# Kernel tuning notes

Measured on AMD Instinct MI355X. Metric: run time of the kernel, lower is better.

The kernel has to match this reference:

```python
import jax, jax.numpy as jnp
import numpy as np

B, E, F, T, RANK, L = 8, 512, 1024, 2048, 10, 5


def setup_inputs() -> dict:
    key = jax.random.key(0)
    ks = jax.random.split(key, 6)
    Y = jax.random.normal(ks[0], (B, E, T), dtype=jnp.float32)
    R = jax.random.uniform(ks[1], (B, E, F), dtype=jnp.float32)
    Omega = (jax.random.uniform(ks[2], (B, E, T)) < 0.9).astype(jnp.float32)
    P0 = jax.random.normal(ks[3], (B, E, RANK), dtype=jnp.float32)
    Q0 = jax.random.normal(ks[4], (B, T, RANK), dtype=jnp.float32)
    A0 = jnp.zeros((B, F, T), dtype=jnp.float32)
    lam_log = jnp.full((L,), -5.0, dtype=jnp.float32)   # init_val=-5
    mu_log = jnp.full((L,), -5.0, dtype=jnp.float32)
    skip_logits = jnp.full((L, 3), 0.5, dtype=jnp.float32)  # skip_P, skip_Q, skip_A
    return {"Y": Y, "R": R, "Omega": Omega, "P0": P0, "Q0": Q0, "A0": A0,
            "lam_log": lam_log, "mu_log": mu_log, "skip_logits": skip_logits}


def _soft(x, t):
    return jnp.sign(x) * jnp.maximum(jnp.abs(x) - t, 0.0)


def _forward(Y, R, Omega, P0, Q0, A0, lam_log, mu_log, skip_logits):
    r = P0.shape[-1]
    I = jnp.eye(r, dtype=Y.dtype)

    def step(carry, params):
        P, Q, A = carry
        ll, ml, sk = params
        lam = jnp.exp(ll)   # lam1 == lam2 (two_lambda=False)
        mu = jnp.exp(ml)
        err = Omega * (Y - R @ A)                                   # [B,E,T]
        # --- P update: per-row masked ridge solve ---
        Mp = jnp.einsum('bet,btr,bts->bers', Omega, Q, Q) + lam * I  # [B,E,r,r]
        rhsP = jnp.einsum('bet,btr->ber', err, Q)
        P_hat = jnp.linalg.solve(Mp, rhsP[..., None])[..., 0]
        P_new = P + jax.nn.sigmoid(sk[0]) * (P_hat - P)
        # --- Q update: per-column masked ridge solve (uses P_new, same err) ---
        Mq = jnp.einsum('bet,ber,bes->btrs', Omega, P_new, P_new) + lam * I
        rhsQ = jnp.einsum('bet,ber->btr', err, P_new)
        Q_hat = jnp.linalg.solve(Mq, rhsQ[..., None])[..., 0]
        Q_new = Q + jax.nn.sigmoid(sk[1]) * (Q_hat - Q)
        # --- A update: soft-thresholded BSCA step ---
        datafit = Omega * (Y - P_new @ jnp.swapaxes(Q_new, -2, -1) - R @ A)
        A_scale = jnp.einsum('bef,bet->bft', R * R, Omega)          # [B,F,T]
        BA_temp = A_scale * A + jnp.einsum('bef,bet->bft', R, datafit)
        zero = A_scale == 0
        denom = jnp.where(zero, 1.0, A_scale)
        A_hat = jnp.where(zero, 0.0, _soft(BA_temp, mu) / denom)
        A_new = A + jax.nn.sigmoid(sk[2]) * (A_hat - A)
        return (P_new, Q_new, A_new), None

    (P, Q, A), _ = jax.lax.scan(step, (P0, Q0, A0), (lam_log, mu_log, skip_logits))
    return P, Q, A


def reference(Y, R, Omega, P0, Q0, A0, lam_log, mu_log, skip_logits):
    return _forward(Y, R, Omega, P0, Q0, A0, lam_log, mu_log, skip_logits)
```

## Files before the change

kernel.cpp:

```cpp
#include <hip/hip_runtime.h>

constexpr int B_ = 8, E_ = 512, F_ = 1024, T_ = 2048, R_ = 10, L_ = 5;
constexpr int NTRI = 55;
constexpr int BM_ = 128, BN_ = 256, BK_ = 32;

enum { EPI_STORE = 0, EPI_ERR = 1, EPI_AUPD = 2, EPI_AUPD0 = 3 };

typedef __attribute__((ext_vector_type(4))) float f32x4;
typedef __attribute__((ext_vector_type(8))) short short8v;
union U8 { unsigned u[4]; short8v s; };

__device__ __forceinline__ unsigned bf16r(float v) {
  unsigned u = __float_as_uint(v);
  return (u + 0x7fffu + ((u >> 16) & 1u)) >> 16;
}
__device__ __forceinline__ unsigned pack1(float v) {
  unsigned h = bf16r(v);
  float lo = v - __uint_as_float(h << 16);
  return h | (bf16r(lo) << 16);
}
__device__ __forceinline__ uint4 pack4(float4 v) {
  uint4 r;
  r.x = pack1(v.x); r.y = pack1(v.y); r.z = pack1(v.z); r.w = pack1(v.w);
  return r;
}
__device__ __forceinline__ void unpack8(uint4 w0, uint4 w1, U8& hi, U8& lo) {
  hi.u[0] = __builtin_amdgcn_perm(w0.y, w0.x, 0x05040100u);
  lo.u[0] = __builtin_amdgcn_perm(w0.y, w0.x, 0x07060302u);
  hi.u[1] = __builtin_amdgcn_perm(w0.w, w0.z, 0x05040100u);
  lo.u[1] = __builtin_amdgcn_perm(w0.w, w0.z, 0x07060302u);
  hi.u[2] = __builtin_amdgcn_perm(w1.y, w1.x, 0x05040100u);
  lo.u[2] = __builtin_amdgcn_perm(w1.y, w1.x, 0x07060302u);
  hi.u[3] = __builtin_amdgcn_perm(w1.w, w1.z, 0x05040100u);
  lo.u[3] = __builtin_amdgcn_perm(w1.w, w1.z, 0x07060302u);
}

__device__ __forceinline__ float sigmoidf_(float v) {
  return 1.0f / (1.0f + expf(-v));
}

__device__ __forceinline__ void solve10(float M[NTRI], const float rhs[R_],
                                        float lam, float x[R_]) {
#pragma unroll
  for (int j = 0; j < R_; j++) M[j * (j + 1) / 2 + j] += lam;
#pragma unroll
  for (int j = 0; j < R_; j++) {
    float s = M[j * (j + 1) / 2 + j];
#pragma unroll
    for (int k = 0; k < j; k++) {
      float l = M[j * (j + 1) / 2 + k];
      s -= l * l;
    }
    s = fmaxf(s, 1e-30f);
    float d = sqrtf(s);
    float inv = 1.0f / d;
    M[j * (j + 1) / 2 + j] = d;
#pragma unroll
    for (int i = j + 1; i < R_; i++) {
      float s2 = M[i * (i + 1) / 2 + j];
#pragma unroll
      for (int k = 0; k < j; k++)
        s2 -= M[i * (i + 1) / 2 + k] * M[j * (j + 1) / 2 + k];
      M[i * (i + 1) / 2 + j] = s2 * inv;
    }
  }
  float y[R_];
#pragma unroll
  for (int i = 0; i < R_; i++) {
    float s = rhs[i];
#pragma unroll
    for (int k = 0; k < i; k++) s -= M[i * (i + 1) / 2 + k] * y[k];
    y[i] = s / M[i * (i + 1) / 2 + i];
  }
#pragma unroll
  for (int ii = R_ - 1; ii >= 0; ii--) {
    float s = y[ii];
#pragma unroll
    for (int k = ii + 1; k < R_; k++) s -= M[k * (k + 1) / 2 + ii] * x[k];
    x[ii] = s / M[ii * (ii + 1) / 2 + ii];
  }
}

template <int MODE>
__global__ __launch_bounds__(256) void trans_k(const float* __restrict__ in0,
                                               const float* __restrict__ in1,
                                               float* __restrict__ out, int Rw,
                                               int Cl) {
  __shared__ float tile[32][36];
  long ib = (long)blockIdx.z * Rw * Cl;
  int r0 = blockIdx.y * 32, c0 = blockIdx.x * 32;
  int tid = threadIdx.x;
  int c4 = (tid & 7) << 2, r = tid >> 3;
  float4 v = *(const float4*)(in0 + ib + (long)(r0 + r) * Cl + c0 + c4);
  if (MODE == 1) {
    float4 w = *(const float4*)(in1 + ib + (long)(r0 + r) * Cl + c0 + c4);
    v.x *= w.x; v.y *= w.y; v.z *= w.z; v.w *= w.w;
  }
  *(float4*)&tile[r][c4] = v;
  __syncthreads();
  int co = tid >> 3, ro4 = (tid & 7) << 2;
  float4 o;
  o.x = tile[ro4 + 0][co];
  o.y = tile[ro4 + 1][co];
  o.z = tile[ro4 + 2][co];
  o.w = tile[ro4 + 3][co];
  *(float4*)(out + ib + (long)(c0 + co) * Rw + r0 + ro4) = o;
}

template <int EPI, int SQB>
__global__ __launch_bounds__(256, 2) void gemm_split(
    const float* __restrict__ Ag, const float* __restrict__ Bg,
    float* __restrict__ Cg, const float* __restrict__ aux1,
    const float* __restrict__ aux2, const float* __restrict__ mu_log,
    const float* __restrict__ sk, int step, int M, int N, int K, long sA,
    long sB, long sC) {
  __shared__ unsigned As[BM_ * BK_];
  __shared__ unsigned Bs[BN_ * BK_];
  int b = blockIdx.z;
  const float* A = Ag + (long)b * sA;
  const float* Bop = Bg + (long)b * sB;
  float* C = Cg + (long)b * sC;
  const float* x1 = aux1 ? aux1 + (long)b * sC : nullptr;
  const float* x2 = aux2 ? aux2 + (long)b * sC : nullptr;

  int tid = threadIdx.x;
  int m0 = blockIdx.y * BM_, n0 = blockIdx.x * BN_;
  int g = tid & 7, rb = tid >> 3;
  int g4 = g << 2;
  int l = tid & 63, lr = l & 15, lh = l >> 4;
  int wv = tid >> 6, wr = wv >> 1, wc = wv & 1;

  f32x4 acc[4][8];
#pragma unroll
  for (int i = 0; i < 4; i++)
#pragma unroll
    for (int j = 0; j < 8; j++) acc[i][j] = {0.f, 0.f, 0.f, 0.f};

  float4 va[4], vb[8];
#pragma unroll
  for (int p = 0; p < 4; p++)
    va[p] = *(const float4*)&A[(long)(m0 + rb + 32 * p) * K + g4];
#pragma unroll
  for (int p = 0; p < 8; p++)
    vb[p] = *(const float4*)&Bop[(long)(n0 + rb + 32 * p) * K + g4];

  for (int kt = 0; kt < K; kt += BK_) {
    uint4 pa[4], pb[8];
#pragma unroll
    for (int p = 0; p < 4; p++) pa[p] = pack4(va[p]);
#pragma unroll
    for (int p = 0; p < 8; p++) {
      float4 v = vb[p];
      if (SQB) { v.x *= v.x; v.y *= v.y; v.z *= v.z; v.w *= v.w; }
      pb[p] = pack4(v);
    }
    __syncthreads();
#pragma unroll
    for (int p = 0; p < 4; p++) {
      int row = rb + 32 * p;
      *(uint4*)&As[row * BK_ + ((g ^ (row & 7)) << 2)] = pa[p];
    }
#pragma unroll
    for (int p = 0; p < 8; p++) {
      int row = rb + 32 * p;
      *(uint4*)&Bs[row * BK_ + ((g ^ (row & 7)) << 2)] = pb[p];
    }
    __syncthreads();
    if (kt + BK_ < K) {
#pragma unroll
      for (int p = 0; p < 4; p++)
        va[p] = *(const float4*)&A[(long)(m0 + rb + 32 * p) * K + kt + BK_ + g4];
#pragma unroll
      for (int p = 0; p < 8; p++)
        vb[p] = *(const float4*)&Bop[(long)(n0 + rb + 32 * p) * K + kt + BK_ + g4];
    }
    U8 aH[4], aL[4];
#pragma unroll
    for (int mf = 0; mf < 4; mf++) {
      int m = wr * 64 + mf * 16 + lr;
      int s7 = m & 7, g0 = 2 * lh;
      uint4 w0 = *(const uint4*)&As[m * BK_ + ((g0 ^ s7) << 2)];
      uint4 w1 = *(const uint4*)&As[m * BK_ + (((g0 + 1) ^ s7) << 2)];
      unpack8(w0, w1, aH[mf], aL[mf]);
    }
#pragma unroll
    for (int nf = 0; nf < 8; nf++) {
      int n = wc * 128 + nf * 16 + lr;
      int s7 = n & 7, g0 = 2 * lh;
      uint4 w0 = *(const uint4*)&Bs[n * BK_ + ((g0 ^ s7) << 2)];
      uint4 w1 = *(const uint4*)&Bs[n * BK_ + (((g0 + 1) ^ s7) << 2)];
      U8 bH, bL;
      unpack8(w0, w1, bH, bL);
#pragma unroll
      for (int mf = 0; mf < 4; mf++) {
        acc[mf][nf] = __builtin_amdgcn_mfma_f32_16x16x32_bf16(
            aH[mf].s, bH.s, acc[mf][nf], 0, 0, 0);
        acc[mf][nf] = __builtin_amdgcn_mfma_f32_16x16x32_bf16(
            aL[mf].s, bH.s, acc[mf][nf], 0, 0, 0);
        acc[mf][nf] = __builtin_amdgcn_mfma_f32_16x16x32_bf16(
            aH[mf].s, bL.s, acc[mf][nf], 0, 0, 0);
      }
    }
  }

  float mu = 0.f, s2 = 0.f;
  if (EPI == EPI_AUPD || EPI == EPI_AUPD0) {
    mu = expf(mu_log[step]);
    s2 = sigmoidf_(sk[step * 3 + 2]);
  }
#pragma unroll
  for (int mf = 0; mf < 4; mf++) {
#pragma unroll
    for (int nf = 0; nf < 8; nf++) {
#pragma unroll
      for (int r = 0; r < 4; r++) {
        int m = m0 + wr * 64 + mf * 16 + lh * 4 + r;
        int n = n0 + wc * 128 + nf * 16 + lr;
        long idx = (long)m * N + n;
        float c = acc[mf][nf][r];
        if (EPI == EPI_STORE) {
          C[idx] = c;
        } else if (EPI == EPI_ERR) {
          C[idx] = x1[idx] - x2[idx] * c;
        } else {
          float asv = x1[idx];
          float aold = (EPI == EPI_AUPD) ? C[idx] : 0.f;
          float bat = fmaf(asv, aold, c);
          float mag = fmaxf(fabsf(bat) - mu, 0.f);
          float sft = copysignf(mag, bat);
          float ahat = (asv == 0.f) ? 0.f : sft / asv;
          C[idx] = aold + s2 * (ahat - aold);
        }
      }
    }
  }
}

__global__ __launch_bounds__(256) void p_stage1(const float* __restrict__ errT,
                                                const float* __restrict__ OmT,
                                                const float* __restrict__ Q,
                                                float* __restrict__ scr) {
  int tc = blockIdx.x, eb = blockIdx.y, b = blockIdx.z;
  int e = eb * 256 + threadIdx.x;
  float Ms[NTRI], rhs[R_];
#pragma unroll
  for (int i = 0; i < NTRI; i++) Ms[i] = 0.f;
#pragma unroll
  for (int i = 0; i < R_; i++) rhs[i] = 0.f;
  long base = (long)b * T_ * E_ + e;
  for (int t = tc * 128; t < tc * 128 + 128; ++t) {
    const float* qr = Q + ((long)b * T_ + t) * R_;
    float q[R_];
#pragma unroll
    for (int r = 0; r < R_; r++) q[r] = qr[r];
    float w = OmT[base + (long)t * E_];
    float ev = errT[base + (long)t * E_];
    float wq[R_];
#pragma unroll
    for (int r = 0; r < R_; r++) {
      wq[r] = w * q[r];
      rhs[r] = fmaf(ev, q[r], rhs[r]);
    }
    int idx = 0;
#pragma unroll
    for (int r = 0; r < R_; r++)
#pragma unroll
      for (int s = 0; s <= r; s++) {
        Ms[idx] = fmaf(wq[r], q[s], Ms[idx]);
        idx++;
      }
  }
  long so = ((long)b * 16 + tc) * 65 * E_ + e;
#pragma unroll
  for (int i = 0; i < NTRI; i++) scr[so + (long)i * E_] = Ms[i];
#pragma unroll
  for (int i = 0; i < R_; i++) scr[so + (long)(NTRI + i) * E_] = rhs[i];
}

__global__ __launch_bounds__(256) void p_stage2(
    const float* __restrict__ scr, const float* __restrict__ Pin,
    float* __restrict__ Pout, const float* __restrict__ lam_log,
    const float* __restrict__ sk, int step) {
  int idx = blockIdx.x * 256 + threadIdx.x;
  int b = idx >> 9, e = idx & 511;
  float Ms[NTRI], rhs[R_], x[R_];
#pragma unroll
  for (int i = 0; i < NTRI; i++) Ms[i] = 0.f;
#pragma unroll
  for (int i = 0; i < R_; i++) rhs[i] = 0.f;
  for (int tc = 0; tc < 16; ++tc) {
    long so = ((long)b * 16 + tc) * 65 * E_ + e;
#pragma unroll
    for (int i = 0; i < NTRI; i++) Ms[i] += scr[so + (long)i * E_];
#pragma unroll
    for (int i = 0; i < R_; i++) rhs[i] += scr[so + (long)(NTRI + i) * E_];
  }
  float lam = expf(lam_log[step]);
  solve10(Ms, rhs, lam, x);
  float s0 = sigmoidf_(sk[step * 3 + 0]);
#pragma unroll
  for (int r = 0; r < R_; r++) {
    float pold = Pin[(long)idx * R_ + r];
    Pout[(long)idx * R_ + r] = pold + s0 * (x[r] - pold);
  }
}

__global__ __launch_bounds__(256) void q_stage1(const float* __restrict__ errT,
                                                const float* __restrict__ OmT,
                                                const float* __restrict__ Pn,
                                                float* __restrict__ scr) {
  int ec = blockIdx.x, tb = blockIdx.y, b = blockIdx.z;
  int t = tb * 256 + threadIdx.x;
  float Ms[NTRI], rhs[R_];
#pragma unroll
  for (int i = 0; i < NTRI; i++) Ms[i] = 0.f;
#pragma unroll
  for (int i = 0; i < R_; i++) rhs[i] = 0.f;
  long base = ((long)b * T_ + t) * E_;
  for (int e = ec * 128; e < ec * 128 + 128; ++e) {
    const float* pr = Pn + ((long)b * E_ + e) * R_;
    float p[R_];
#pragma unroll
    for (int r = 0; r < R_; r++) p[r] = pr[r];
    float w = OmT[base + e];
    float ev = errT[base + e];
    float wp[R_];
#pragma unroll
    for (int r = 0; r < R_; r++) {
      wp[r] = w * p[r];
      rhs[r] = fmaf(ev, p[r], rhs[r]);
    }
    int idx = 0;
#pragma unroll
    for (int r = 0; r < R_; r++)
#pragma unroll
      for (int s = 0; s <= r; s++) {
        Ms[idx] = fmaf(wp[r], p[s], Ms[idx]);
        idx++;
      }
  }
  long so = ((long)b * 4 + ec) * 65 * T_ + t;
#pragma unroll
  for (int i = 0; i < NTRI; i++) scr[so + (long)i * T_] = Ms[i];
#pragma unroll
  for (int i = 0; i < R_; i++) scr[so + (long)(NTRI + i) * T_] = rhs[i];
}

__global__ __launch_bounds__(256) void q_stage2(
    const float* __restrict__ scr, const float* __restrict__ Qin,
    float* __restrict__ Qout, const float* __restrict__ lam_log,
    const float* __restrict__ sk, int step) {
  int idx = blockIdx.x * 256 + threadIdx.x;
  int b = idx >> 11, t = idx & 2047;
  float Ms[NTRI], rhs[R_], x[R_];
#pragma unroll
  for (int i = 0; i < NTRI; i++) Ms[i] = 0.f;
#pragma unroll
  for (int i = 0; i < R_; i++) rhs[i] = 0.f;
  for (int ec = 0; ec < 4; ++ec) {
    long so = ((long)b * 4 + ec) * 65 * T_ + t;
#pragma unroll
    for (int i = 0; i < NTRI; i++) Ms[i] += scr[so + (long)i * T_];
#pragma unroll
    for (int i = 0; i < R_; i++) rhs[i] += scr[so + (long)(NTRI + i) * T_];
  }
  float lam = expf(lam_log[step]);
  solve10(Ms, rhs, lam, x);
  float s1 = sigmoidf_(sk[step * 3 + 1]);
#pragma unroll
  for (int r = 0; r < R_; r++) {
    float qold = Qin[(long)idx * R_ + r];
    Qout[(long)idx * R_ + r] = qold + s1 * (x[r] - qold);
  }
}

__global__ __launch_bounds__(256) void datafit_k(
    const float* __restrict__ errIn, float* __restrict__ errOut,
    const float* __restrict__ OmT, const float* __restrict__ Pn,
    const float* __restrict__ Qn) {
  int tc = blockIdx.x, eb = blockIdx.y, b = blockIdx.z;
  int e = eb * 256 + threadIdx.x;
  float p[R_];
#pragma unroll
  for (int r = 0; r < R_; r++) p[r] = Pn[((long)b * E_ + e) * R_ + r];
  for (int t = tc * 16; t < tc * 16 + 16; ++t) {
    const float* qr = Qn + ((long)b * T_ + t) * R_;
    float dot = 0.f;
#pragma unroll
    for (int r = 0; r < R_; r++) dot = fmaf(p[r], qr[r], dot);
    long ix = ((long)b * T_ + t) * E_ + e;
    errOut[ix] = errIn[ix] - OmT[ix] * dot;
  }
}

extern "C" void kernel_launch(void* const* d_in, const int* in_sizes, int n_in,
                              void* d_out, int out_size, void* d_ws,
                              size_t ws_size, hipStream_t stream) {
  const float* Y = (const float*)d_in[0];
  const float* Rm = (const float*)d_in[1];
  const float* Om = (const float*)d_in[2];
  const float* P0 = (const float*)d_in[3];
  const float* Q0 = (const float*)d_in[4];
  const float* lam_log = (const float*)d_in[6];
  const float* mu_log = (const float*)d_in[7];
  const float* sk = (const float*)d_in[8];

  float* ws = (float*)d_ws;
  float* OmT = ws;
  float* YOm = OmT + (long)B_ * T_ * E_;
  float* errT = YOm + (long)B_ * T_ * E_;
  float* AscT = errT + (long)B_ * T_ * E_;
  float* Rt = AscT + (long)B_ * T_ * F_;
  float* Pa = Rt + (long)B_ * F_ * E_;
  float* Pb = Pa + B_ * E_ * R_;
  float* Qa = Pb + B_ * E_ * R_;
  float* Qb = Qa + B_ * T_ * R_;
  float* scr = Qb + B_ * T_ * R_;

  float* outP = (float*)d_out;
  float* outQ = outP + B_ * E_ * R_;
  float* AT = outQ + B_ * T_ * R_;

  const float* Pr[L_] = {P0, Pa, Pb, Pa, Pb};
  float* Pw[L_] = {Pa, Pb, Pa, Pb, outP};
  const float* Qr[L_] = {Q0, Qa, Qb, Qa, Qb};
  float* Qw[L_] = {Qa, Qb, Qa, Qb, outQ};

  dim3 blk(256);
  trans_k<0><<<dim3(T_ / 32, E_ / 32, B_), blk, 0, stream>>>(Om, nullptr, OmT,
                                                             E_, T_);
  trans_k<1><<<dim3(T_ / 32, E_ / 32, B_), blk, 0, stream>>>(Y, Om, YOm, E_,
                                                             T_);
  trans_k<0><<<dim3(F_ / 32, E_ / 32, B_), blk, 0, stream>>>(Rm, nullptr, Rt,
                                                             E_, F_);
  gemm_split<EPI_STORE, 1><<<dim3(F_ / BN_, T_ / BM_, B_), blk, 0, stream>>>(
      OmT, Rt, AscT, nullptr, nullptr, nullptr, nullptr, 0, T_, F_, E_,
      (long)T_ * E_, (long)F_ * E_, (long)T_ * F_);

  for (int s = 0; s < L_; ++s) {
    const float* errS = (s == 0) ? YOm : errT;
    if (s > 0) {
      gemm_split<EPI_ERR, 0><<<dim3(E_ / BN_, T_ / BM_, B_), blk, 0, stream>>>(
          AT, Rm, errT, YOm, OmT, nullptr, nullptr, s, T_, E_, F_,
          (long)T_ * F_, (long)E_ * F_, (long)T_ * E_);
    }
    p_stage1<<<dim3(16, 2, B_), blk, 0, stream>>>(errS, OmT, Qr[s], scr);
    p_stage2<<<16, blk, 0, stream>>>(scr, Pr[s], Pw[s], lam_log, sk, s);
    q_stage1<<<dim3(4, 8, B_), blk, 0, stream>>>(errS, OmT, Pw[s], scr);
    q_stage2<<<64, blk, 0, stream>>>(scr, Qr[s], Qw[s], lam_log, sk, s);
    datafit_k<<<dim3(128, 2, B_), blk, 0, stream>>>(errS, errT, OmT, Pw[s],
                                                    Qw[s]);
    if (s == 0)
      gemm_split<EPI_AUPD0, 0>
          <<<dim3(F_ / BN_, T_ / BM_, B_), blk, 0, stream>>>(
              errT, Rt, AT, AscT, nullptr, mu_log, sk, s, T_, F_, E_,
              (long)T_ * E_, (long)F_ * E_, (long)T_ * F_);
    else
      gemm_split<EPI_AUPD, 0><<<dim3(F_ / BN_, T_ / BM_, B_), blk, 0, stream>>>(
          errT, Rt, AT, AscT, nullptr, mu_log, sk, s, T_, F_, E_,
          (long)T_ * E_, (long)F_ * E_, (long)T_ * F_);
  }
  for (int b = 0; b < B_; ++b) {
    trans_k<0><<<dim3(F_ / 32, T_ / 32, 1), blk, 0, stream>>>(
        AT + (long)b * T_ * F_, nullptr, scr, T_, F_);
    hipMemcpyAsync(AT + (long)b * T_ * F_, scr, (long)T_ * F_ * sizeof(float),
                   hipMemcpyDeviceToDevice, stream);
  }
}
```

Before: 2.423 ms.

## Store operands as pre-split bf16 hi/lo pairs and bitpack the mask

Replaces the fp32 workspaces with precomputed bf16 hi/lo split arrays for Y, err, R, R^T, R^2 and A. The GEMMs then load ready-made MFMA fragments and skip per-tile packing. Omega is bitpacked and A_scale is recomputed inside the A-update GEMM as an extra MFMA accumulation, so the A_scale buffer is gone. The final per-batch transpose plus memcpy becomes a single transpose kernel. This cuts memory traffic and conversion work, at the cost of extra MFMAs per tile and storing A with reduced-precision hi/lo.

After: 3.793 ms. 56.6% more time.

```diff
diff --git a/kernel.cpp b/kernel.cpp
--- a/kernel.cpp
+++ b/kernel.cpp
@@ -2,39 +2,24 @@
 
 constexpr int B_ = 8, E_ = 512, F_ = 1024, T_ = 2048, R_ = 10, L_ = 5;
 constexpr int NTRI = 55;
-constexpr int BM_ = 128, BN_ = 256, BK_ = 32;
-
-enum { EPI_STORE = 0, EPI_ERR = 1, EPI_AUPD = 2, EPI_AUPD0 = 3 };
+constexpr int EW = E_ / 32;
 
 typedef __attribute__((ext_vector_type(4))) float f32x4;
 typedef __attribute__((ext_vector_type(8))) short short8v;
-union U8 { unsigned u[4]; short8v s; };
-
-__device__ __forceinline__ unsigned bf16r(float v) {
+
+__device__ __forceinline__ float bf2f(unsigned short h) {
+  return __uint_as_float(((unsigned)h) << 16);
+}
+__device__ __forceinline__ unsigned short f2bf(float v) {
   unsigned u = __float_as_uint(v);
-  return (u + 0x7fffu + ((u >> 16) & 1u)) >> 16;
-}
-__device__ __forceinline__ unsigned pack1(float v) {
-  unsigned h = bf16r(v);
-  float lo = v - __uint_as_float(h << 16);
-  return h | (bf16r(lo) << 16);
-}
-__device__ __forceinline__ uint4 pack4(float4 v) {
-  uint4 r;
-  r.x = pack1(v.x); r.y = pack1(v.y); r.z = pack1(v.z); r.w = pack1(v.w);
-  return r;
-}
-__device__ __forceinline__ void unpack8(uint4 w0, uint4 w1, U8& hi, U8& lo) {
-  hi.u[0] = __builtin_amdgcn_perm(w0.y, w0.x, 0x05040100u);
-  lo.u[0] = __builtin_amdgcn_perm(w0.y, w0.x, 0x07060302u);
-  hi.u[1] = __builtin_amdgcn_perm(w0.w, w0.z, 0x05040100u);
-  lo.u[1] = __builtin_amdgcn_perm(w0.w, w0.z, 0x07060302u);
-  hi.u[2] = __builtin_amdgcn_perm(w1.y, w1.x, 0x05040100u);
-  lo.u[2] = __builtin_amdgcn_perm(w1.y, w1.x, 0x07060302u);
-  hi.u[3] = __builtin_amdgcn_perm(w1.w, w1.z, 0x05040100u);
-  lo.u[3] = __builtin_amdgcn_perm(w1.w, w1.z, 0x07060302u);
-}
-
+  u = u + 0x7fffu + ((u >> 16) & 1u);
+  return (unsigned short)(u >> 16);
+}
+__device__ __forceinline__ void split2(float v, unsigned short& h,
+                                       unsigned short& l) {
+  h = f2bf(v);
+  l = f2bf(v - bf2f(h));
+}
 __device__ __forceinline__ float sigmoidf_(float v) {
   return 1.0f / (1.0f + expf(-v));
 }
@@ -81,22 +66,551 @@
   }
 }
 
-template <int MODE>
-__global__ __launch_bounds__(256) void trans_k(const float* __restrict__ in0,
-                                               const float* __restrict__ in1,
-                                               float* __restrict__ out, int Rw,
-                                               int Cl) {
-  __shared__ float tile[32][36];
-  long ib = (long)blockIdx.z * Rw * Cl;
-  int r0 = blockIdx.y * 32, c0 = blockIdx.x * 32;
+__global__ __launch_bounds__(256, 2) void gemm_err(
+    const unsigned short* __restrict__ AHp, const unsigned short* __restrict__ ALp,
+    const unsigned short* __restrict__ BHp, const unsigned short* __restrict__ BLp,
+    const unsigned short* __restrict__ YHp, const unsigned short* __restrict__ YLp,
+    const unsigned* __restrict__ omb, unsigned short* __restrict__ eHp,
+    unsigned short* __restrict__ eLp) {
+  constexpr int K = F_;
+  __shared__ unsigned short AsH[4096], AsL[4096], BsH[4096], BsL[4096];
+  int b = blockIdx.z, tid = threadIdx.x;
+  int m0 = blockIdx.y * 128, n0 = blockIdx.x * 128;
+  const unsigned short* AH = AHp + (long)b * T_ * F_;
+  const unsigned short* AL = ALp + (long)b * T_ * F_;
+  const unsigned short* BH = BHp + (long)b * E_ * F_;
+  const unsigned short* BL = BLp + (long)b * E_ * F_;
+  int lr = tid & 15, lh = (tid >> 4) & 3, wv = tid >> 6, wr = wv >> 1,
+      wc = wv & 1;
+  int srow = tid >> 2, sslot = tid & 3;
+
+  f32x4 acc[4][4];
+#pragma unroll
+  for (int i = 0; i < 4; i++)
+#pragma unroll
+    for (int j = 0; j < 4; j++) acc[i][j] = {0.f, 0.f, 0.f, 0.f};
+
+  uint4 ld[8];
+#pragma unroll
+  for (int j = 0; j < 2; j++) {
+    ld[j] = *(const uint4*)&AH[(long)(m0 + srow + 64 * j) * K + sslot * 8];
+    ld[2 + j] = *(const uint4*)&AL[(long)(m0 + srow + 64 * j) * K + sslot * 8];
+    ld[4 + j] = *(const uint4*)&BH[(long)(n0 + srow + 64 * j) * K + sslot * 8];
+    ld[6 + j] = *(const uint4*)&BL[(long)(n0 + srow + 64 * j) * K + sslot * 8];
+  }
+  for (int kt = 0; kt < K; kt += 32) {
+#pragma unroll
+    for (int j = 0; j < 2; j++) {
+      int li = (srow + 64 * j) * 32 + sslot * 8;
+      *(uint4*)&AsH[li] = ld[j];
+      *(uint4*)&AsL[li] = ld[2 + j];
+      *(uint4*)&BsH[li] = ld[4 + j];
+      *(uint4*)&BsL[li] = ld[6 + j];
+    }
+    __syncthreads();
+    if (kt + 32 < K) {
+      int k1 = kt + 32;
+#pragma unroll
+      for (int j = 0; j < 2; j++) {
+        ld[j] = *(const uint4*)&AH[(long)(m0 + srow + 64 * j) * K + k1 + sslot * 8];
+        ld[2 + j] = *(const uint4*)&AL[(long)(m0 + srow + 64 * j) * K + k1 + sslot * 8];
+        ld[4 + j] = *(const uint4*)&BH[(long)(n0 + srow + 64 * j) * K + k1 + sslot * 8];
+        ld[6 + j] = *(const uint4*)&BL[(long)(n0 + srow + 64 * j) * K + k1 + sslot * 8];
+      }
+    }
+    short8v aH[4], aL[4];
+#pragma unroll
+    for (int mf = 0; mf < 4; mf++) {
+      int ml = wr * 64 + mf * 16 + lr;
+      aH[mf] = *(const short8v*)&AsH[ml * 32 + lh * 8];
+      aL[mf] = *(const short8v*)&AsL[ml * 32 + lh * 8];
+    }
+#pragma unroll
+    for (int nf = 0; nf < 4; nf++) {
+      int nl = wc * 64 + nf * 16 + lr;
+      short8v bH = *(const short8v*)&BsH[nl * 32 + lh * 8];
+      short8v bL = *(const short8v*)&BsL[nl * 32 + lh * 8];
+#pragma unroll
+      for (int mf = 0; mf < 4; mf++) {
+        acc[mf][nf] = __builtin_amdgcn_mfma_f32_16x16x32_bf16(aH[mf], bH,
+                                                              acc[mf][nf], 0, 0, 0);
+        acc[mf][nf] = __builtin_amdgcn_mfma_f32_16x16x32_bf16(aH[mf], bL,
+                                                              acc[mf][nf], 0, 0, 0);
+        acc[mf][nf] = __builtin_amdgcn_mfma_f32_16x16x32_bf16(aL[mf], bH,
+                                                              acc[mf][nf], 0, 0, 0);
+      }
+    }
+    __syncthreads();
+  }
+#pragma unroll
+  for (int mf = 0; mf < 4; mf++)
+#pragma unroll
+    for (int nf = 0; nf < 4; nf++)
+#pragma unroll
+      for (int r = 0; r < 4; r++) {
+        int m = m0 + wr * 64 + mf * 16 + lh * 4 + r;
+        int n = n0 + wc * 64 + nf * 16 + lr;
+        long row = (long)b * T_ + m;
+        long idx = row * E_ + n;
+        float y = bf2f(YHp[idx]) + bf2f(YLp[idx]);
+        unsigned w = omb[row * EW + (n >> 5)];
+        float om = ((w >> (n & 31)) & 1) ? 1.f : 0.f;
+        float er = y - om * acc[mf][nf][r];
+        unsigned short h, l;
+        split2(er, h, l);
+        eHp[idx] = h;
+        eLp[idx] = l;
+      }
+}
+
+template <int S0>
+__global__ __launch_bounds__(256, 2) void gemm_aupd(
+    const unsigned short* __restrict__ eHp, const unsigned short* __restrict__ eLp,
+    const unsigned* __restrict__ omb, const unsigned short* __restrict__ RtHp,
+    const unsigned short* __restrict__ RtLp, const unsigned short* __restrict__ R2Hp,
+    const unsigned short* __restrict__ R2Lp,
+    unsigned short* __restrict__ AHp, unsigned short* __restrict__ ALp,
+    const float* __restrict__ mu_log, const float* __restrict__ sk, int step) {
+  constexpr int K = E_;
+  __shared__ unsigned short AsH[4096], AsL[4096], AsO[4096], BsH[4096],
+      BsL[4096], Bs2[4096], Bs2L[4096];
+  int b = blockIdx.z, tid = threadIdx.x;
+  int m0 = blockIdx.y * 128, n0 = blockIdx.x * 128;
+  const unsigned short* eH = eHp + (long)b * T_ * E_;
+  const unsigned short* eL = eLp + (long)b * T_ * E_;
+  const unsigned short* BH = RtHp + (long)b * F_ * E_;
+  const unsigned short* BL = RtLp + (long)b * F_ * E_;
+  const unsigned short* B2 = R2Hp + (long)b * F_ * E_;
+  const unsigned short* B2L = R2Lp + (long)b * F_ * E_;
+  int lr = tid & 15, lh = (tid >> 4) & 3, wv = tid >> 6, wr = wv >> 1,
+      wc = wv & 1;
+  int srow = tid >> 2, sslot = tid & 3;
+
+  f32x4 accC[4][4], accS[4][4];
+#pragma unroll
+  for (int i = 0; i < 4; i++)
+#pragma unroll
+    for (int j = 0; j < 4; j++) {
+      accC[i][j] = {0.f, 0.f, 0.f, 0.f};
+      accS[i][j] = {0.f, 0.f, 0.f, 0.f};
+    }
+
+  uint4 ld[12];
+  unsigned ow[2];
+#pragma unroll
+  for (int j = 0; j < 2; j++) {
+    long ar = (long)b * T_ + m0 + srow + 64 * j;
+    ld[j] = *(const uint4*)&eH[(long)(m0 + srow + 64 * j) * K + sslot * 8];
+    ld[2 + j] = *(const uint4*)&eL[(long)(m0 + srow + 64 * j) * K + sslot * 8];
+    ow[j] = omb[ar * EW + 0];
+    ld[4 + j] = *(const uint4*)&BH[(long)(n0 + srow + 64 * j) * K + sslot * 8];
+    ld[6 + j] = *(const uint4*)&BL[(long)(n0 + srow + 64 * j) * K + sslot * 8];
+    ld[8 + j] = *(const uint4*)&B2[(long)(n0 + srow + 64 * j) * K + sslot * 8];
+    ld[10 + j] = *(const uint4*)&B2L[(long)(n0 + srow + 64 * j) * K + sslot * 8];
+  }
+  for (int kt = 0; kt < K; kt += 32) {
+#pragma unroll
+    for (int j = 0; j < 2; j++) {
+      int li = (srow + 64 * j) * 32 + sslot * 8;
+      *(uint4*)&AsH[li] = ld[j];
+      *(uint4*)&AsL[li] = ld[2 + j];
+      union { unsigned short us[8]; uint4 v; } ob;
+#pragma unroll
+      for (int i = 0; i < 8; i++)
+        ob.us[i] = ((ow[j] >> (sslot * 8 + i)) & 1) ? (unsigned short)0x3f80 : 0;
+      *(uint4*)&AsO[li] = ob.v;
+      *(uint4*)&BsH[li] = ld[4 + j];
+      *(uint4*)&BsL[li] = ld[6 + j];
+      *(uint4*)&Bs2[li] = ld[8 + j];
+      *(uint4*)&Bs2L[li] = ld[10 + j];
+    }
+    __syncthreads();
+    if (kt + 32 < K) {
+      int k1 = kt + 32;
+#pragma unroll
+      for (int j = 0; j < 2; j++) {
+        long ar = (long)b * T_ + m0 + srow + 64 * j;
+        ld[j] = *(const uint4*)&eH[(long)(m0 + srow + 64 * j) * K + k1 + sslot * 8];
+        ld[2 + j] = *(const uint4*)&eL[(long)(m0 + srow + 64 * j) * K + k1 + sslot * 8];
+        ow[j] = omb[ar * EW + (k1 >> 5)];
+        ld[4 + j] = *(const uint4*)&BH[(long)(n0 + srow + 64 * j) * K + k1 + sslot * 8];
+        ld[6 + j] = *(const uint4*)&BL[(long)(n0 + srow + 64 * j) * K + k1 + sslot * 8];
+        ld[8 + j] = *(const uint4*)&B2[(long)(n0 + srow + 64 * j) * K + k1 + sslot * 8];
+        ld[10 + j] = *(const uint4*)&B2L[(long)(n0 + srow + 64 * j) * K + k1 + sslot * 8];
+      }
+    }
+    {
+      short8v aH[4], aL[4];
+#pragma unroll
+      for (int mf = 0; mf < 4; mf++) {
+        int ml = wr * 64 + mf * 16 + lr;
+        aH[mf] = *(const short8v*)&AsH[ml * 32 + lh * 8];
+        aL[mf] = *(const short8v*)&AsL[ml * 32 + lh * 8];
+      }
+#pragma unroll
+      for (int nf = 0; nf < 4; nf++) {
+        int nl = wc * 64 + nf * 16 + lr;
+        short8v bH = *(const short8v*)&BsH[nl * 32 + lh * 8];
+        short8v bL = *(const short8v*)&BsL[nl * 32 + lh * 8];
+#pragma unroll
+        for (int mf = 0; mf < 4; mf++) {
+          accC[mf][nf] = __builtin_amdgcn_mfma_f32_16x16x32_bf16(
+              aH[mf], bH, accC[mf][nf], 0, 0, 0);
+          accC[mf][nf] = __builtin_amdgcn_mfma_f32_16x16x32_bf16(
+              aH[mf], bL, accC[mf][nf], 0, 0, 0);
+          accC[mf][nf] = __builtin_amdgcn_mfma_f32_16x16x32_bf16(
+              aL[mf], bH, accC[mf][nf], 0, 0, 0);
+        }
+      }
+    }
+    {
+      short8v aO[4];
+#pragma unroll
+      for (int mf = 0; mf < 4; mf++) {
+        int ml = wr * 64 + mf * 16 + lr;
+        aO[mf] = *(const short8v*)&AsO[ml * 32 + lh * 8];
+      }
+#pragma unroll
+      for (int nf = 0; nf < 4; nf++) {
+        int nl = wc * 64 + nf * 16 + lr;
+        short8v b2 = *(const short8v*)&Bs2[nl * 32 + lh * 8];
+        short8v b2l = *(const short8v*)&Bs2L[nl * 32 + lh * 8];
+#pragma unroll
+        for (int mf = 0; mf < 4; mf++) {
+          accS[mf][nf] = __builtin_amdgcn_mfma_f32_16x16x32_bf16(
+              aO[mf], b2, accS[mf][nf], 0, 0, 0);
+          accS[mf][nf] = __builtin_amdgcn_mfma_f32_16x16x32_bf16(
+              aO[mf], b2l, accS[mf][nf], 0, 0, 0);
+        }
+      }
+    }
+    __syncthreads();
+  }
+  float mu = expf(mu_log[step]);
+  float s2 = sigmoidf_(sk[step * 3 + 2]);
+#pragma unroll
+  for (int mf = 0; mf < 4; mf++)
+#pragma unroll
+    for (int nf = 0; nf < 4; nf++)
+#pragma unroll
+      for (int r = 0; r < 4; r++) {
+        int m = m0 + wr * 64 + mf * 16 + lh * 4 + r;
+        int n = n0 + wc * 64 + nf * 16 + lr;
+        long idx = ((long)b * T_ + m) * F_ + n;
+        float asc = accS[mf][nf][r];
+        float c = accC[mf][nf][r];
+        float aold = S0 ? 0.f : (bf2f(AHp[idx]) + bf2f(ALp[idx]));
+        float bat = fmaf(asc, aold, c);
+        float mag = fmaxf(fabsf(bat) - mu, 0.f);
+        float sft = copysignf(mag, bat);
+        float ahat = (asc == 0.f) ? 0.f : sft / asc;
+        float anew = aold + s2 * (ahat - aold);
+        unsigned short h, l;
+        split2(anew, h, l);
+        AHp[idx] = h;
+        ALp[idx] = l;
+      }
+}
+
+__global__ __launch_bounds__(256) void p_stage1(
+    const unsigned short* __restrict__ eH, const unsigned short* __restrict__ eL,
+    const unsigned* __restrict__ omb, const float* __restrict__ Q,
+    float* __restrict__ scr) {
+  int tc = blockIdx.x, eb = blockIdx.y, b = blockIdx.z;
+  int e = eb * 256 + threadIdx.x;
+  float Ms[NTRI], rhs[R_];
+#pragma unroll
+  for (int i = 0; i < NTRI; i++) Ms[i] = 0.f;
+#pragma unroll
+  for (int i = 0; i < R_; i++) rhs[i] = 0.f;
+  for (int t = tc * 128; t < tc * 128 + 128; ++t) {
+    const float* qr = Q + ((long)b * T_ + t) * R_;
+    float q[R_];
+#pragma unroll
+    for (int r = 0; r < R_; r++) q[r] = qr[r];
+    long row = (long)b * T_ + t;
+    long ix = row * E_ + e;
+    float ev = bf2f(eH[ix]) + bf2f(eL[ix]);
+    unsigned w = omb[row * EW + (e >> 5)];
+    float wv = ((w >> (e & 31)) & 1) ? 1.f : 0.f;
+    float wq[R_];
+#pragma unroll
+    for (int r = 0; r < R_; r++) {
+      wq[r] = wv * q[r];
+      rhs[r] = fmaf(ev, q[r], rhs[r]);
+    }
+    int idx = 0;
+#pragma unroll
+    for (int r = 0; r < R_; r++)
+#pragma unroll
+      for (int s = 0; s <= r; s++) {
+        Ms[idx] = fmaf(wq[r], q[s], Ms[idx]);
+        idx++;
+      }
+  }
+  long so = ((long)b * 16 + tc) * 65 * E_ + e;
+#pragma unroll
+  for (int i = 0; i < NTRI; i++) scr[so + (long)i * E_] = Ms[i];
+#pragma unroll
+  for (int i = 0; i < R_; i++) scr[so + (long)(NTRI + i) * E_] = rhs[i];
+}
+
+__global__ __launch_bounds__(256) void p_stage2(
+    const float* __restrict__ scr, const float* __restrict__ Pin,
+    float* __restrict__ Pout, const float* __restrict__ lam_log,
+    const float* __restrict__ sk, int step) {
+  int idx = blockIdx.x * 256 + threadIdx.x;
+  int b = idx >> 9, e = idx & 511;
+  float Ms[NTRI], rhs[R_], x[R_];
+#pragma unroll
+  for (int i = 0; i < NTRI; i++) Ms[i] = 0.f;
+#pragma unroll
+  for (int i = 0; i < R_; i++) rhs[i] = 0.f;
+  for (int tc = 0; tc < 16; ++tc) {
+    long so = ((long)b * 16 + tc) * 65 * E_ + e;
+#pragma unroll
+    for (int i = 0; i < NTRI; i++) Ms[i] += scr[so + (long)i * E_];
+#pragma unroll
+    for (int i = 0; i < R_; i++) rhs[i] += scr[so + (long)(NTRI + i) * E_];
+  }
+  float lam = expf(lam_log[step]);
+  solve10(Ms, rhs, lam, x);
+  float s0 = sigmoidf_(sk[step * 3 + 0]);
+#pragma unroll
+  for (int r = 0; r < R_; r++) {
+    float pold = Pin[(long)idx * R_ + r];
+    Pout[(long)idx * R_ + r] = pold + s0 * (x[r] - pold);
+  }
+}
+
+__global__ __launch_bounds__(256) void q_stage1(
+    const unsigned short* __restrict__ eH, const unsigned short* __restrict__ eL,
+    const unsigned* __restrict__ omb, const float* __restrict__ Pn,
+    float* __restrict__ scr) {
+  __shared__ float et[256][17], ot[256][17];
+  int ec = blockIdx.x, tb = blockIdx.y, b = blockIdx.z;
+  int tid = threadIdx.x;
+  int t = tb * 256 + tid;
+  float Ms[NTRI], rhs[R_];
+#pragma unroll
+  for (int i = 0; i < NTRI; i++) Ms[i] = 0.f;
+#pragma unroll
+  for (int i = 0; i < R_; i++) rhs[i] = 0.f;
+  int eq = tid & 3, tl = tid >> 2;
+  for (int ch = 0; ch < 8; ++ch) {
+    int e0 = ec * 128 + ch * 16;
+    __syncthreads();
+#pragma unroll
+    for (int p = 0; p < 4; p++) {
+      int ts = tl + 64 * p;
+      long row = (long)b * T_ + tb * 256 + ts;
+      long ix = row * E_ + e0 + eq * 4;
+      ushort4 hv = *(const ushort4*)&eH[ix];
+      ushort4 lv = *(const ushort4*)&eL[ix];
+      unsigned w = omb[row * EW + ((e0 + eq * 4) >> 5)];
+      int bb = (e0 + eq * 4) & 31;
+      et[ts][eq * 4 + 0] = bf2f(hv.x) + bf2f(lv.x);
+      et[ts][eq * 4 + 1] = bf2f(hv.y) + bf2f(lv.y);
+      et[ts][eq * 4 + 2] = bf2f(hv.z) + bf2f(lv.z);
+      et[ts][eq * 4 + 3] = bf2f(hv.w) + bf2f(lv.w);
+      ot[ts][eq * 4 + 0] = ((w >> (bb + 0)) & 1) ? 1.f : 0.f;
+      ot[ts][eq * 4 + 1] = ((w >> (bb + 1)) & 1) ? 1.f : 0.f;
+      ot[ts][eq * 4 + 2] = ((w >> (bb + 2)) & 1) ? 1.f : 0.f;
+      ot[ts][eq * 4 + 3] = ((w >> (bb + 3)) & 1) ? 1.f : 0.f;
+    }
+    __syncthreads();
+    for (int ee = 0; ee < 16; ++ee) {
+      int e = e0 + ee;
+      const float* pr = Pn + ((long)b * E_ + e) * R_;
+      float p10[R_];
+#pragma unroll
+      for (int r = 0; r < R_; r++) p10[r] = pr[r];
+      float wv = ot[tid][ee], ev = et[tid][ee];
+      float wp[R_];
+#pragma unroll
+      for (int r = 0; r < R_; r++) {
+        wp[r] = wv * p10[r];
+        rhs[r] = fmaf(ev, p10[r], rhs[r]);
+      }
+      int idx = 0;
+#pragma unroll
+      for (int r = 0; r < R_; r++)
+#pragma unroll
+        for (int s = 0; s <= r; s++) {
+          Ms[idx] = fmaf(wp[r], p10[s], Ms[idx]);
+          idx++;
+        }
+    }
+  }
+  long so = ((long)b * 4 + ec) * 65 * T_ + t;
+#pragma unroll
+  for (int i = 0; i < NTRI; i++) scr[so + (long)i * T_] = Ms[i];
+#pragma unroll
+  for (int i = 0; i < R_; i++) scr[so + (long)(NTRI + i) * T_] = rhs[i];
+}
+
+__global__ __launch_bounds__(256) void q_stage2(
+    const float* __restrict__ scr, const float* __restrict__ Qin,
+    float* __restrict__ Qout, const float* __restrict__ lam_log,
+    const float* __restrict__ sk, int step) {
+  int idx = blockIdx.x * 256 + threadIdx.x;
+  int b = idx >> 11, t = idx & 2047;
+  float Ms[NTRI], rhs[R_];
+#pragma unroll
+  for (int i = 0; i < NTRI; i++) Ms[i] = 0.f;
+#pragma unroll
+  for (int i = 0; i < R_; i++) rhs[i] = 0.f;
+  for (int ec = 0; ec < 4; ++ec) {
+    long so = ((long)b * 4 + ec) * 65 * T_ + t;
+#pragma unroll
+    for (int i = 0; i < NTRI; i++) Ms[i] += scr[so + (long)i * T_];
+#pragma unroll
+    for (int i = 0; i < R_; i++) rhs[i] += scr[so + (long)(NTRI + i) * T_];
+  }
+  float lam = expf(lam_log[step]);
+  float x2[R_];
+  solve10(Ms, rhs, lam, x2);
+  float s1 = sigmoidf_(sk[step * 3 + 1]);
+#pragma unroll
+  for (int r = 0; r < R_; r++) {
+    float qold = Qin[(long)idx * R_ + r];
+    Qout[(long)idx * R_ + r] = qold + s1 * (x2[r] - qold);
+  }
+}
+
+__global__ __launch_bounds__(256) void datafit_k(
+    const unsigned short* __restrict__ inH, const unsigned short* __restrict__ inL,
+    unsigned short* __restrict__ outH, unsigned short* __restrict__ outL,
+    const unsigned* __restrict__ omb, const float* __restrict__ Pn,
+    const float* __restrict__ Qn) {
+  int tc = blockIdx.x, eb = blockIdx.y, b = blockIdx.z;
+  int e = eb * 256 + threadIdx.x;
+  float p[R_];
+#pragma unroll
+  for (int r = 0; r < R_; r++) p[r] = Pn[((long)b * E_ + e) * R_ + r];
+  for (int t = tc * 16; t < tc * 16 + 16; ++t) {
+    const float* qr = Qn + ((long)b * T_ + t) * R_;
+    float dot = 0.f;
+#pragma unroll
+    for (int r = 0; r < R_; r++) dot = fmaf(p[r], qr[r], dot);
+    long row = (long)b * T_ + t;
+    long ix = row * E_ + e;
+    unsigned w = omb[row * EW + (e >> 5)];
+    float om = ((w >> (e & 31)) & 1) ? 1.f : 0.f;
+    float er = (bf2f(inH[ix]) + bf2f(inL[ix])) - om * dot;
+    unsigned short h, l;
+    split2(er, h, l);
+    outH[ix] = h;
+    outL[ix] = l;
+  }
+}
+
+__global__ __launch_bounds__(256) void bitpack_om(const float* __restrict__ Om,
+                                                  unsigned* __restrict__ omb) {
+  __shared__ float tl[128][65];
+  int t0 = blockIdx.x * 64, e0 = blockIdx.y * 128, b = blockIdx.z;
+  int tid = threadIdx.x;
+  for (int j = 0; j < 32; j++) {
+    int idx = tid + 256 * j;
+    int el = idx >> 6, tloc = idx & 63;
+    tl[el][tloc] = Om[((long)b * E_ + e0 + el) * T_ + t0 + tloc];
+  }
+  __syncthreads();
+  int tloc = tid & 63, wg = tid >> 6;
+  unsigned w = 0;
+  for (int i = 0; i < 32; i++)
+    w |= (tl[wg * 32 + i][tloc] != 0.f ? 1u : 0u) << i;
+  omb[((long)b * T_ + t0 + tloc) * EW + e0 / 32 + wg] = w;
+}
+
+__global__ __launch_bounds__(256) void transpack_y(
+    const float* __restrict__ Y, const float* __restrict__ Om,
+    unsigned short* __restrict__ YH, unsigned short* __restrict__ YL) {
+  __shared__ float tile[32][33];
+  int c0 = blockIdx.x * 32, r0 = blockIdx.y * 32, b = blockIdx.z;
   int tid = threadIdx.x;
   int c4 = (tid & 7) << 2, r = tid >> 3;
-  float4 v = *(const float4*)(in0 + ib + (long)(r0 + r) * Cl + c0 + c4);
-  if (MODE == 1) {
-    float4 w = *(const float4*)(in1 + ib + (long)(r0 + r) * Cl + c0 + c4);
-    v.x *= w.x; v.y *= w.y; v.z *= w.z; v.w *= w.w;
-  }
-  *(float4*)&tile[r][c4] = v;
+  long ib = (long)b * E_ * T_;
+  float4 v = *(const float4*)&Y[ib + (long)(r0 + r) * T_ + c0 + c4];
+  float4 w = *(const float4*)&Om[ib + (long)(r0 + r) * T_ + c0 + c4];
+  tile[r][c4 + 0] = v.x * w.x;
+  tile[r][c4 + 1] = v.y * w.y;
+  tile[r][c4 + 2] = v.z * w.z;
+  tile[r][c4 + 3] = v.w * w.w;
+  __syncthreads();
+  int co = tid >> 3, ro4 = (tid & 7) << 2;
+  ushort4 h, l;
+  split2(tile[ro4 + 0][co], h.x, l.x);
+  split2(tile[ro4 + 1][co], h.y, l.y);
+  split2(tile[ro4 + 2][co], h.z, l.z);
+  split2(tile[ro4 + 3][co], h.w, l.w);
+  long ob = ((long)b * T_ + c0 + co) * E_ + r0 + ro4;
+  *(ushort4*)&YH[ob] = h;
+  *(ushort4*)&YL[ob] = l;
+}
+
+__global__ __launch_bounds__(256) void transpack_r(
+    const float* __restrict__ Rm, unsigned short* __restrict__ RtH,
+    unsigned short* __restrict__ RtL, unsigned short* __restrict__ R2H,
+    unsigned short* __restrict__ R2L) {
+  __shared__ float tile[32][33];
+  int c0 = blockIdx.x * 32, r0 = blockIdx.y * 32, b = blockIdx.z;
+  int tid = threadIdx.x;
+  int c4 = (tid & 7) << 2, r = tid >> 3;
+  long ib = (long)b * E_ * F_;
+  float4 v = *(const float4*)&Rm[ib + (long)(r0 + r) * F_ + c0 + c4];
+  tile[r][c4 + 0] = v.x;
+  tile[r][c4 + 1] = v.y;
+  tile[r][c4 + 2] = v.z;
+  tile[r][c4 + 3] = v.w;
+  __syncthreads();
+  int co = tid >> 3, ro4 = (tid & 7) << 2;
+  ushort4 h, l, s, sl;
+  float a0 = tile[ro4 + 0][co], a1 = tile[ro4 + 1][co];
+  float a2 = tile[ro4 + 2][co], a3 = tile[ro4 + 3][co];
+  split2(a0, h.x, l.x);
+  split2(a1, h.y, l.y);
+  split2(a2, h.z, l.z);
+  split2(a3, h.w, l.w);
+  split2(a0 * a0, s.x, sl.x);
+  split2(a1 * a1, s.y, sl.y);
+  split2(a2 * a2, s.z, sl.z);
+  split2(a3 * a3, s.w, sl.w);
+  long ob = ((long)b * F_ + c0 + co) * E_ + r0 + ro4;
+  *(ushort4*)&RtH[ob] = h;
+  *(ushort4*)&RtL[ob] = l;
+  *(ushort4*)&R2H[ob] = s;
+  *(ushort4*)&R2L[ob] = sl;
+}
+
+__global__ __launch_bounds__(256) void pack_rm(const float* __restrict__ Rm,
+                                               unsigned short* __restrict__ RmH,
+                                               unsigned short* __restrict__ RmL) {
+  long i = ((long)blockIdx.x * 256 + threadIdx.x) * 4;
+  float4 v = *(const float4*)&Rm[i];
+  ushort4 h, l;
+  split2(v.x, h.x, l.x);
+  split2(v.y, h.y, l.y);
+  split2(v.z, h.z, l.z);
+  split2(v.w, h.w, l.w);
+  *(ushort4*)&RmH[i] = h;
+  *(ushort4*)&RmL[i] = l;
+}
+
+__global__ __launch_bounds__(256) void trans_out(
+    const unsigned short* __restrict__ AH, const unsigned short* __restrict__ AL,
+    float* __restrict__ outA) {
+  __shared__ float tile[32][33];
+  int c0 = blockIdx.x * 32, r0 = blockIdx.y * 32, b = blockIdx.z;
+  int tid = threadIdx.x;
+  int c4 = (tid & 7) << 2, r = tid >> 3;
+  long ib = (long)b * T_ * F_;
+  ushort4 h = *(const ushort4*)&AH[ib + (long)(r0 + r) * F_ + c0 + c4];
+  ushort4 l = *(const ushort4*)&AL[ib + (long)(r0 + r) * F_ + c0 + c4];
+  tile[r][c4 + 0] = bf2f(h.x) + bf2f(l.x);
+  tile[r][c4 + 1] = bf2f(h.y) + bf2f(l.y);
+  tile[r][c4 + 2] = bf2f(h.z) + bf2f(l.z);
+  tile[r][c4 + 3] = bf2f(h.w) + bf2f(l.w);
   __syncthreads();
   int co = tid >> 3, ro4 = (tid & 7) << 2;
   float4 o;
@@ -104,293 +618,7 @@
   o.y = tile[ro4 + 1][co];
   o.z = tile[ro4 + 2][co];
   o.w = tile[ro4 + 3][co];
-  *(float4*)(out + ib + (long)(c0 + co) * Rw + r0 + ro4) = o;
-}
-
-template <int EPI, int SQB>
-__global__ __launch_bounds__(256, 2) void gemm_split(
-    const float* __restrict__ Ag, const float* __restrict__ Bg,
-    float* __restrict__ Cg, const float* __restrict__ aux1,
-    const float* __restrict__ aux2, const float* __restrict__ mu_log,
-    const float* __restrict__ sk, int step, int M, int N, int K, long sA,
-    long sB, long sC) {
-  __shared__ unsigned As[BM_ * BK_];
-  __shared__ unsigned Bs[BN_ * BK_];
-  int b = blockIdx.z;
-  const float* A = Ag + (long)b * sA;
-  const float* Bop = Bg + (long)b * sB;
-  float* C = Cg + (long)b * sC;
-  const float* x1 = aux1 ? aux1 + (long)b * sC : nullptr;
-  const float* x2 = aux2 ? aux2 + (long)b * sC : nullptr;
-
-  int tid = threadIdx.x;
-  int m0 = blockIdx.y * BM_, n0 = blockIdx.x * BN_;
-  int g = tid & 7, rb = tid >> 3;
-  int g4 = g << 2;
-  int l = tid & 63, lr = l & 15, lh = l >> 4;
-  int wv = tid >> 6, wr = wv >> 1, wc = wv & 1;
-
-  f32x4 acc[4][8];
-#pragma unroll
-  for (int i = 0; i < 4; i++)
-#pragma unroll
-    for (int j = 0; j < 8; j++) acc[i][j] = {0.f, 0.f, 0.f, 0.f};
-
-  float4 va[4], vb[8];
-#pragma unroll
-  for (int p = 0; p < 4; p++)
-    va[p] = *(const float4*)&A[(long)(m0 + rb + 32 * p) * K + g4];
-#pragma unroll
-  for (int p = 0; p < 8; p++)
-    vb[p] = *(const float4*)&Bop[(long)(n0 + rb + 32 * p) * K + g4];
-
-  for (int kt = 0; kt < K; kt += BK_) {
-    uint4 pa[4], pb[8];
-#pragma unroll
-    for (int p = 0; p < 4; p++) pa[p] = pack4(va[p]);
-#pragma unroll
-    for (int p = 0; p < 8; p++) {
-      float4 v = vb[p];
-      if (SQB) { v.x *= v.x; v.y *= v.y; v.z *= v.z; v.w *= v.w; }
-      pb[p] = pack4(v);
-    }
-    __syncthreads();
-#pragma unroll
-    for (int p = 0; p < 4; p++) {
-      int row = rb + 32 * p;
-      *(uint4*)&As[row * BK_ + ((g ^ (row & 7)) << 2)] = pa[p];
-    }
-#pragma unroll
-    for (int p = 0; p < 8; p++) {
-      int row = rb + 32 * p;
-      *(uint4*)&Bs[row * BK_ + ((g ^ (row & 7)) << 2)] = pb[p];
-    }
-    __syncthreads();
-    if (kt + BK_ < K) {
-#pragma unroll
-      for (int p = 0; p < 4; p++)
-        va[p] = *(const float4*)&A[(long)(m0 + rb + 32 * p) * K + kt + BK_ + g4];
-#pragma unroll
-      for (int p = 0; p < 8; p++)
-        vb[p] = *(const float4*)&Bop[(long)(n0 + rb + 32 * p) * K + kt + BK_ + g4];
-    }
-    U8 aH[4], aL[4];
-#pragma unroll
-    for (int mf = 0; mf < 4; mf++) {
-      int m = wr * 64 + mf * 16 + lr;
-      int s7 = m & 7, g0 = 2 * lh;
-      uint4 w0 = *(const uint4*)&As[m * BK_ + ((g0 ^ s7) << 2)];
-      uint4 w1 = *(const uint4*)&As[m * BK_ + (((g0 + 1) ^ s7) << 2)];
-      unpack8(w0, w1, aH[mf], aL[mf]);
-    }
-#pragma unroll
-    for (int nf = 0; nf < 8; nf++) {
-      int n = wc * 128 + nf * 16 + lr;
-      int s7 = n & 7, g0 = 2 * lh;
-      uint4 w0 = *(const uint4*)&Bs[n * BK_ + ((g0 ^ s7) << 2)];
-      uint4 w1 = *(const uint4*)&Bs[n * BK_ + (((g0 + 1) ^ s7) << 2)];
-      U8 bH, bL;
-      unpack8(w0, w1, bH, bL);
-#pragma unroll
-      for (int mf = 0; mf < 4; mf++) {
-        acc[mf][nf] = __builtin_amdgcn_mfma_f32_16x16x32_bf16(
-            aH[mf].s, bH.s, acc[mf][nf], 0, 0, 0);
-        acc[mf][nf] = __builtin_amdgcn_mfma_f32_16x16x32_bf16(
-            aL[mf].s, bH.s, acc[mf][nf], 0, 0, 0);
-        acc[mf][nf] = __builtin_amdgcn_mfma_f32_16x16x32_bf16(
-            aH[mf].s, bL.s, acc[mf][nf], 0, 0, 0);
-      }
-    }
-  }
-
-  float mu = 0.f, s2 = 0.f;
-  if (EPI == EPI_AUPD || EPI == EPI_AUPD0) {
-    mu = expf(mu_log[step]);
-    s2 = sigmoidf_(sk[step * 3 + 2]);
-  }
-#pragma unroll
-  for (int mf = 0; mf < 4; mf++) {
-#pragma unroll
-    for (int nf = 0; nf < 8; nf++) {
-#pragma unroll
-      for (int r = 0; r < 4; r++) {
-        int m = m0 + wr * 64 + mf * 16 + lh * 4 + r;
-        int n = n0 + wc * 128 + nf * 16 + lr;
-        long idx = (long)m * N + n;
-        float c = acc[mf][nf][r];
-        if (EPI == EPI_STORE) {
-          C[idx] = c;
-        } else if (EPI == EPI_ERR) {
-          C[idx] = x1[idx] - x2[idx] * c;
-        } else {
-          float asv = x1[idx];
-          float aold = (EPI == EPI_AUPD) ? C[idx] : 0.f;
-          float bat = fmaf(asv, aold, c);
-          float mag = fmaxf(fabsf(bat) - mu, 0.f);
-          float sft = copysignf(mag, bat);
-          float ahat = (asv == 0.f) ? 0.f : sft / asv;
-          C[idx] = aold + s2 * (ahat - aold);
-        }
-      }
-    }
-  }
-}
-
-__global__ __launch_bounds__(256) void p_stage1(const float* __restrict__ errT,
-                                                const float* __restrict__ OmT,
-                                                const float* __restrict__ Q,
-                                                float* __restrict__ scr) {
-  int tc = blockIdx.x, eb = blockIdx.y, b = blockIdx.z;
-  int e = eb * 256 + threadIdx.x;
-  float Ms[NTRI], rhs[R_];
-#pragma unroll
-  for (int i = 0; i < NTRI; i++) Ms[i] = 0.f;
-#pragma unroll
-  for (int i = 0; i < R_; i++) rhs[i] = 0.f;
-  long base = (long)b * T_ * E_ + e;
-  for (int t = tc * 128; t < tc * 128 + 128; ++t) {
-    const float* qr = Q + ((long)b * T_ + t) * R_;
-    float q[R_];
-#pragma unroll
-    for (int r = 0; r < R_; r++) q[r] = qr[r];
-    float w = OmT[base + (long)t * E_];
-    float ev = errT[base + (long)t * E_];
-    float wq[R_];
-#pragma unroll
-    for (int r = 0; r < R_; r++) {
-      wq[r] = w * q[r];
-      rhs[r] = fmaf(ev, q[r], rhs[r]);
-    }
-    int idx = 0;
-#pragma unroll
-    for (int r = 0; r < R_; r++)
-#pragma unroll
-      for (int s = 0; s <= r; s++) {
-        Ms[idx] = fmaf(wq[r], q[s], Ms[idx]);
-        idx++;
-      }
-  }
-  long so = ((long)b * 16 + tc) * 65 * E_ + e;
-#pragma unroll
-  for (int i = 0; i < NTRI; i++) scr[so + (long)i * E_] = Ms[i];
-#pragma unroll
-  for (int i = 0; i < R_; i++) scr[so + (long)(NTRI + i) * E_] = rhs[i];
-}
-
-__global__ __launch_bounds__(256) void p_stage2(
-    const float* __restrict__ scr, const float* __restrict__ Pin,
-    float* __restrict__ Pout, const float* __restrict__ lam_log,
-    const float* __restrict__ sk, int step) {
-  int idx = blockIdx.x * 256 + threadIdx.x;
-  int b = idx >> 9, e = idx & 511;
-  float Ms[NTRI], rhs[R_], x[R_];
-#pragma unroll
-  for (int i = 0; i < NTRI; i++) Ms[i] = 0.f;
-#pragma unroll
-  for (int i = 0; i < R_; i++) rhs[i] = 0.f;
-  for (int tc = 0; tc < 16; ++tc) {
-    long so = ((long)b * 16 + tc) * 65 * E_ + e;
-#pragma unroll
-    for (int i = 0; i < NTRI; i++) Ms[i] += scr[so + (long)i * E_];
-#pragma unroll
-    for (int i = 0; i < R_; i++) rhs[i] += scr[so + (long)(NTRI + i) * E_];
-  }
-  float lam = expf(lam_log[step]);
-  solve10(Ms, rhs, lam, x);
-  float s0 = sigmoidf_(sk[step * 3 + 0]);
-#pragma unroll
-  for (int r = 0; r < R_; r++) {
-    float pold = Pin[(long)idx * R_ + r];
-    Pout[(long)idx * R_ + r] = pold + s0 * (x[r] - pold);
-  }
-}
-
-__global__ __launch_bounds__(256) void q_stage1(const float* __restrict__ errT,
-                                                const float* __restrict__ OmT,
-                                                const float* __restrict__ Pn,
-                                                float* __restrict__ scr) {
-  int ec = blockIdx.x, tb = blockIdx.y, b = blockIdx.z;
-  int t = tb * 256 + threadIdx.x;
-  float Ms[NTRI], rhs[R_];
-#pragma unroll
-  for (int i = 0; i < NTRI; i++) Ms[i] = 0.f;
-#pragma unroll
-  for (int i = 0; i < R_; i++) rhs[i] = 0.f;
-  long base = ((long)b * T_ + t) * E_;
-  for (int e = ec * 128; e < ec * 128 + 128; ++e) {
-    const float* pr = Pn + ((long)b * E_ + e) * R_;
-    float p[R_];
-#pragma unroll
-    for (int r = 0; r < R_; r++) p[r] = pr[r];
-    float w = OmT[base + e];
-    float ev = errT[base + e];
-    float wp[R_];
-#pragma unroll
-    for (int r = 0; r < R_; r++) {
-      wp[r] = w * p[r];
-      rhs[r] = fmaf(ev, p[r], rhs[r]);
-    }
-    int idx = 0;
-#pragma unroll
-    for (int r = 0; r < R_; r++)
-#pragma unroll
-      for (int s = 0; s <= r; s++) {
-        Ms[idx] = fmaf(wp[r], p[s], Ms[idx]);
-        idx++;
-      }
-  }
-  long so = ((long)b * 4 + ec) * 65 * T_ + t;
-#pragma unroll
-  for (int i = 0; i < NTRI; i++) scr[so + (long)i * T_] = Ms[i];
-#pragma unroll
-  for (int i = 0; i < R_; i++) scr[so + (long)(NTRI + i) * T_] = rhs[i];
-}
-
-__global__ __launch_bounds__(256) void q_stage2(
-    const float* __restrict__ scr, const float* __restrict__ Qin,
-    float* __restrict__ Qout, const float* __restrict__ lam_log,
-    const float* __restrict__ sk, int step) {
-  int idx = blockIdx.x * 256 + threadIdx.x;
-  int b = idx >> 11, t = idx & 2047;
-  float Ms[NTRI], rhs[R_], x[R_];
-#pragma unroll
-  for (int i = 0; i < NTRI; i++) Ms[i] = 0.f;
-#pragma unroll
-  for (int i = 0; i < R_; i++) rhs[i] = 0.f;
-  for (int ec = 0; ec < 4; ++ec) {
-    long so = ((long)b * 4 + ec) * 65 * T_ + t;
-#pragma unroll
-    for (int i = 0; i < NTRI; i++) Ms[i] += scr[so + (long)i * T_];
-#pragma unroll
-    for (int i = 0; i < R_; i++) rhs[i] += scr[so + (long)(NTRI + i) * T_];
-  }
-  float lam = expf(lam_log[step]);
-  solve10(Ms, rhs, lam, x);
-  float s1 = sigmoidf_(sk[step * 3 + 1]);
-#pragma unroll
-  for (int r = 0; r < R_; r++) {
-    float qold = Qin[(long)idx * R_ + r];
-    Qout[(long)idx * R_ + r] = qold + s1 * (x[r] - qold);
-  }
-}
-
-__global__ __launch_bounds__(256) void datafit_k(
-    const float* __restrict__ errIn, float* __restrict__ errOut,
-    const float* __restrict__ OmT, const float* __restrict__ Pn,
-    const float* __restrict__ Qn) {
-  int tc = blockIdx.x, eb = blockIdx.y, b = blockIdx.z;
-  int e = eb * 256 + threadIdx.x;
-  float p[R_];
-#pragma unroll
-  for (int r = 0; r < R_; r++) p[r] = Pn[((long)b * E_ + e) * R_ + r];
-  for (int t = tc * 16; t < tc * 16 + 16; ++t) {
-    const float* qr = Qn + ((long)b * T_ + t) * R_;
-    float dot = 0.f;
-#pragma unroll
-    for (int r = 0; r < R_; r++) dot = fmaf(p[r], qr[r], dot);
-    long ix = ((long)b * T_ + t) * E_ + e;
-    errOut[ix] = errIn[ix] - OmT[ix] * dot;
-  }
+  *(float4*)&outA[(long)b * F_ * T_ + (long)(c0 + co) * T_ + r0 + ro4] = o;
 }
 
 extern "C" void kernel_launch(void* const* d_in, const int* in_sizes, int n_in,
@@ -405,21 +633,29 @@
   const float* mu_log = (const float*)d_in[7];
   const float* sk = (const float*)d_in[8];
 
-  float* ws = (float*)d_ws;
-  float* OmT = ws;
-  float* YOm = OmT + (long)B_ * T_ * E_;
-  float* errT = YOm + (long)B_ * T_ * E_;
-  float* AscT = errT + (long)B_ * T_ * E_;
-  float* Rt = AscT + (long)B_ * T_ * F_;
-  float* Pa = Rt + (long)B_ * F_ * E_;
-  float* Pb = Pa + B_ * E_ * R_;
-  float* Qa = Pb + B_ * E_ * R_;
-  float* Qb = Qa + B_ * T_ * R_;
-  float* scr = Qb + B_ * T_ * R_;
+  char* w = (char*)d_ws;
+  float* scr = (float*)w;                     w += 17039360;
+  float* Pa = (float*)w;                      w += 163840;
+  float* Pb = (float*)w;                      w += 163840;
+  float* Qa = (float*)w;                      w += 655360;
+  float* Qb = (float*)w;                      w += 655360;
+  unsigned short* YH = (unsigned short*)w;    w += 16777216;
+  unsigned short* YL = (unsigned short*)w;    w += 16777216;
+  unsigned short* eH = (unsigned short*)w;    w += 16777216;
+  unsigned short* eL = (unsigned short*)w;    w += 16777216;
+  unsigned* OmB = (unsigned*)w;               w += 1048576;
+  unsigned short* RmH = (unsigned short*)w;   w += 8388608;
+  unsigned short* RmL = (unsigned short*)w;   w += 8388608;
+  unsigned short* RtH = (unsigned short*)w;   w += 8388608;
+  unsigned short* RtL = (unsigned short*)w;   w += 8388608;
+  unsigned short* R2H = (unsigned short*)w;   w += 8388608;
+  unsigned short* R2L = (unsigned short*)w;   w += 8388608;
+  unsigned short* AH = (unsigned short*)w;    w += 33554432;
+  unsigned short* AL = (unsigned short*)w;    w += 33554432;
 
   float* outP = (float*)d_out;
   float* outQ = outP + B_ * E_ * R_;
-  float* AT = outQ + B_ * T_ * R_;
+  float* outA = outQ + B_ * T_ * R_;
 
   const float* Pr[L_] = {P0, Pa, Pb, Pa, Pb};
   float* Pw[L_] = {Pa, Pb, Pa, Pb, outP};
@@ -427,43 +663,31 @@
   float* Qw[L_] = {Qa, Qb, Qa, Qb, outQ};
 
   dim3 blk(256);
-  trans_k<0><<<dim3(T_ / 32, E_ / 32, B_), blk, 0, stream>>>(Om, nullptr, OmT,
-                                                             E_, T_);
-  trans_k<1><<<dim3(T_ / 32, E_ / 32, B_), blk, 0, stream>>>(Y, Om, YOm, E_,
-                                                             T_);
-  trans_k<0><<<dim3(F_ / 32, E_ / 32, B_), blk, 0, stream>>>(Rm, nullptr, Rt,
-                                                             E_, F_);
-  gemm_split<EPI_STORE, 1><<<dim3(F_ / BN_, T_ / BM_, B_), blk, 0, stream>>>(
-      OmT, Rt, AscT, nullptr, nullptr, nullptr, nullptr, 0, T_, F_, E_,
-      (long)T_ * E_, (long)F_ * E_, (long)T_ * F_);
+  bitpack_om<<<dim3(T_ / 64, E_ / 128, B_), blk, 0, stream>>>(Om, OmB);
+  transpack_y<<<dim3(T_ / 32, E_ / 32, B_), blk, 0, stream>>>(Y, Om, YH, YL);
+  pack_rm<<<(B_ * E_ * F_) / 1024, blk, 0, stream>>>(Rm, RmH, RmL);
+  transpack_r<<<dim3(F_ / 32, E_ / 32, B_), blk, 0, stream>>>(Rm, RtH, RtL,
+                                                              R2H, R2L);
 
   for (int s = 0; s < L_; ++s) {
-    const float* errS = (s == 0) ? YOm : errT;
-    if (s > 0) {
-      gemm_split<EPI_ERR, 0><<<dim3(E_ / BN_, T_ / BM_, B_), blk, 0, stream>>>(
-          AT, Rm, errT, YOm, OmT, nullptr, nullptr, s, T_, E_, F_,
-          (long)T_ * F_, (long)E_ * F_, (long)T_ * E_);
-    }
-    p_stage1<<<dim3(16, 2, B_), blk, 0, stream>>>(errS, OmT, Qr[s], scr);
+    const unsigned short* pH = s ? eH : YH;
+    const unsigned short* pL = s ? eL : YL;
+    if (s) {
+      gemm_err<<<dim3(E_ / 128, T_ / 128, B_), blk, 0, stream>>>(
+          AH, AL, RmH, RmL, YH, YL, OmB, eH, eL);
+    }
+    p_stage1<<<dim3(16, 2, B_), blk, 0, stream>>>(pH, pL, OmB, Qr[s], scr);
     p_stage2<<<16, blk, 0, stream>>>(scr, Pr[s], Pw[s], lam_log, sk, s);
-    q_stage1<<<dim3(4, 8, B_), blk, 0, stream>>>(errS, OmT, Pw[s], scr);
+    q_stage1<<<dim3(4, 8, B_), blk, 0, stream>>>(pH, pL, OmB, Pw[s], scr);
     q_stage2<<<64, blk, 0, stream>>>(scr, Qr[s], Qw[s], lam_log, sk, s);
-    datafit_k<<<dim3(128, 2, B_), blk, 0, stream>>>(errS, errT, OmT, Pw[s],
+    datafit_k<<<dim3(128, 2, B_), blk, 0, stream>>>(pH, pL, eH, eL, OmB, Pw[s],
                                                     Qw[s]);
     if (s == 0)
-      gemm_split<EPI_AUPD0, 0>
-          <<<dim3(F_ / BN_, T_ / BM_, B_), blk, 0, stream>>>(
-              errT, Rt, AT, AscT, nullptr, mu_log, sk, s, T_, F_, E_,
-              (long)T_ * E_, (long)F_ * E_, (long)T_ * F_);
+      gemm_aupd<1><<<dim3(F_ / 128, T_ / 128, B_), blk, 0, stream>>>(
+          eH, eL, OmB, RtH, RtL, R2H, R2L, AH, AL, mu_log, sk, 0);
     else
-      gemm_split<EPI_AUPD, 0><<<dim3(F_ / BN_, T_ / BM_, B_), blk, 0, stream>>>(
-          errT, Rt, AT, AscT, nullptr, mu_log, sk, s, T_, F_, E_,
-          (long)T_ * E_, (long)F_ * E_, (long)T_ * F_);
-  }
-  for (int b = 0; b < B_; ++b) {
-    trans_k<0><<<dim3(F_ / 32, T_ / 32, 1), blk, 0, stream>>>(
-        AT + (long)b * T_ * F_, nullptr, scr, T_, F_);
-    hipMemcpyAsync(AT + (long)b * T_ * F_, scr, (long)T_ * F_ * sizeof(float),
-                   hipMemcpyDeviceToDevice, stream);
-  }
-}
+      gemm_aupd<0><<<dim3(F_ / 128, T_ / 128, B_), blk, 0, stream>>>(
+          eH, eL, OmB, RtH, RtL, R2H, R2L, AH, AL, mu_log, sk, s);
+  }
+  trans_out<<<dim3(F_ / 32, T_ / 32, B_), blk, 0, stream>>>(AH, AL, outA);
+}
```
